# Performance work log

Measured on AMD Instinct MI355X. Metric: run time of the kernel, lower is better.

Reference implementation:

```python
import jax, jax.numpy as jnp
import numpy as np

D_MODEL = 1024
NUM_HEADS = 16
SEQ = 2048
BATCH = 4


def setup_inputs() -> dict:
    key = jax.random.key(0)
    ks = jax.random.split(key, 9)
    d = D_MODEL
    s = 0.02
    return {
        "x": jax.random.normal(ks[0], (BATCH, SEQ, d), dtype=jnp.float32),
        "WQ_w": jax.random.normal(ks[1], (d, d), dtype=jnp.float32) * s,
        "WQ_b": jnp.zeros((d,), dtype=jnp.float32),
        "WK_w": jax.random.normal(ks[2], (d, d), dtype=jnp.float32) * s,
        "WK_b": jnp.zeros((d,), dtype=jnp.float32),
        "WV_w": jax.random.normal(ks[3], (d, d), dtype=jnp.float32) * s,
        "WV_b": jnp.zeros((d,), dtype=jnp.float32),
        "WO_w": jax.random.normal(ks[4], (d, d), dtype=jnp.float32) * s,
        "WO_b": jnp.zeros((d,), dtype=jnp.float32),
    }


def reference(x, WQ_w, WQ_b, WK_w, WK_b, WV_w, WV_b, WO_w, WO_b):
    b, s, d = x.shape
    n = NUM_HEADS
    dk = d // n
    # projections (torch nn.Linear: y = x @ W.T + b)
    Q = x @ WQ_w.T + WQ_b
    K = x @ WK_w.T + WK_b
    V = x @ WV_w.T + WV_b
    # [b, s, n*dk] -> [b, n, s, dk]
    Q = Q.reshape(b, s, n, dk).transpose(0, 2, 1, 3)
    K = K.reshape(b, s, n, dk).transpose(0, 2, 1, 3)
    V = V.reshape(b, s, n, dk).transpose(0, 2, 1, 3)
    scale = 1.0 / jnp.sqrt(jnp.asarray(dk, dtype=Q.dtype))
    scores = jnp.einsum('bnqd,bnkd->bnqk', Q, K) * scale  # [b,n,s,s]
    causal = jnp.tril(jnp.ones((s, s), dtype=bool))
    scores = jnp.where(causal[None, None], scores, -jnp.inf)
    attn = jax.nn.softmax(scores, axis=-1)
    out = jnp.einsum('bnqk,bnkd->bnqd', attn, V)  # [b,n,s,dk]
    out = out.transpose(0, 2, 1, 3).reshape(b, s, d)  # merge heads
    return out @ WO_w.T + WO_b
```

## Files before the change

### kernel.cpp

```cpp
#include <hip/hip_runtime.h>
#include <hip/hip_bf16.h>
#include <stdint.h>

#define D_MODEL 1024
#define NHEAD 16
#define SEQ 2048
#define BATCH 4
#define DK 64
#define QKVSTR 3072

typedef __attribute__((ext_vector_type(8))) short short8;
typedef __attribute__((ext_vector_type(4))) float f32x4;

#if __has_builtin(__builtin_amdgcn_exp2f)
#define EXP2(x) __builtin_amdgcn_exp2f(x)
#else
#define EXP2(x) exp2f(x)
#endif

__device__ inline unsigned short f2bf(float f) {
  unsigned int u = __builtin_bit_cast(unsigned int, f);
  unsigned int r = (u + 0x7fffu + ((u >> 16) & 1u)) >> 16;
  return (unsigned short)r;
}

__device__ inline unsigned int cvt_pk_bf16(float lo, float hi) {
  unsigned int d;
  asm("v_cvt_pk_bf16_f32 %0, %1, %2" : "=v"(d) : "v"(lo), "v"(hi));
  return d;
}

#define GLOAD_LDS16(g, l) \
  __builtin_amdgcn_global_load_lds((const __attribute__((address_space(1))) unsigned int*)(g), \
      (__attribute__((address_space(3))) unsigned int*)(l), 16, 0, 0)

__global__ void cvt_kernel(const float* __restrict__ in, unsigned short* __restrict__ out, int n) {
  int i = (blockIdx.x * 256 + threadIdx.x) * 8;
  if (i >= n) return;
  const float4* p = (const float4*)(in + i);
  float4 a = p[0], b = p[1];
  union { unsigned short u[8]; uint4 v; } r;
  r.u[0] = f2bf(a.x); r.u[1] = f2bf(a.y); r.u[2] = f2bf(a.z); r.u[3] = f2bf(a.w);
  r.u[4] = f2bf(b.x); r.u[5] = f2bf(b.y); r.u[6] = f2bf(b.z); r.u[7] = f2bf(b.w);
  *(uint4*)(out + i) = r.v;
}

__global__ void cvt4_kernel(const float* __restrict__ i0, const float* __restrict__ i1,
                            const float* __restrict__ i2, const float* __restrict__ i3,
                            unsigned short* __restrict__ out, int n) {
  const int by = blockIdx.y;
  const float* in = (by == 0) ? i0 : (by == 1) ? i1 : (by == 2) ? i2 : i3;
  unsigned short* o = out + (size_t)by * n;
  int i = (blockIdx.x * 256 + threadIdx.x) * 8;
  if (i >= n) return;
  const float4* p = (const float4*)(in + i);
  float4 a = p[0], b = p[1];
  union { unsigned short u[8]; uint4 v; } r;
  r.u[0] = f2bf(a.x); r.u[1] = f2bf(a.y); r.u[2] = f2bf(a.z); r.u[3] = f2bf(a.w);
  r.u[4] = f2bf(b.x); r.u[5] = f2bf(b.y); r.u[6] = f2bf(b.z); r.u[7] = f2bf(b.w);
  *(uint4*)(o + i) = r.v;
}

template <typename CT>
__global__ __launch_bounds__(256)
void gemm_bt(const unsigned short* __restrict__ A, const unsigned short* __restrict__ B,
             const float* __restrict__ b0, const float* __restrict__ b1,
             const float* __restrict__ b2, CT* __restrict__ C, int M, int N, int K,
             int qcols, float alphaQ) {
  __shared__ unsigned short As[128 * 64];
  __shared__ unsigned short Bs[128 * 64];
  const int t = threadIdx.x;
  const int l = t & 63;
  const int w = t >> 6;
  const int wr = w >> 1, wc = w & 1;
  const int l15 = l & 15, lg = l >> 4;
  const int m0 = blockIdx.y * 128, n0 = blockIdx.x * 128;

  f32x4 acc[4][4] = {};

  const int srow = t >> 3;
  const int sc8 = t & 7;
  const int kssw = sc8 ^ (srow & 7);

  const unsigned short* ap = A + (size_t)(m0 + srow) * K + kssw * 8;
  const unsigned short* bp = B + (size_t)(n0 + srow) * K + kssw * 8;

  const int nt = K >> 6;
  for (int kt = 0; kt < nt; ++kt) {
    const int k0 = kt * 64;
    #pragma unroll
    for (int j = 0; j < 4; ++j) {
      GLOAD_LDS16(ap + (size_t)(j * 32) * K + k0, &As[(j * 32 + srow) * 64 + sc8 * 8]);
      GLOAD_LDS16(bp + (size_t)(j * 32) * K + k0, &Bs[(j * 32 + srow) * 64 + sc8 * 8]);
    }
    asm volatile("s_waitcnt vmcnt(0)" ::: "memory");
    __builtin_amdgcn_s_barrier();
    __builtin_amdgcn_sched_barrier(0);

    __builtin_amdgcn_s_setprio(1);
    #pragma unroll
    for (int kk = 0; kk < 2; ++kk) {
      short8 af[4], bfr[4];
      #pragma unroll
      for (int m = 0; m < 4; ++m) {
        int row = wr * 64 + m * 16 + l15;
        af[m] = *(const short8*)&As[row * 64 + (((kk * 4 + lg) ^ (row & 7)) * 8)];
      }
      #pragma unroll
      for (int n = 0; n < 4; ++n) {
        int row = wc * 64 + n * 16 + l15;
        bfr[n] = *(const short8*)&Bs[row * 64 + (((kk * 4 + lg) ^ (row & 7)) * 8)];
      }
      #pragma unroll
      for (int m = 0; m < 4; ++m)
        #pragma unroll
        for (int n = 0; n < 4; ++n)
          acc[m][n] = __builtin_amdgcn_mfma_f32_16x16x32_bf16(af[m], bfr[n], acc[m][n], 0, 0, 0);
    }
    __builtin_amdgcn_s_setprio(0);

    __builtin_amdgcn_s_barrier();
    __builtin_amdgcn_sched_barrier(0);
  }

  #pragma unroll
  for (int m = 0; m < 4; ++m) {
    #pragma unroll
    for (int n = 0; n < 4; ++n) {
      int col = n0 + wc * 64 + n * 16 + l15;
      const float* bp2 = (col < 1024) ? b0 : (col < 2048) ? b1 : b2;
      float bz = bp2[col & 1023];
      #pragma unroll
      for (int r = 0; r < 4; ++r) {
        int row = m0 + wr * 64 + m * 16 + lg * 4 + r;
        float v = acc[m][n][r] + bz;
        if (col < qcols) v *= alphaQ;
        if constexpr (sizeof(CT) == 2) {
          C[(size_t)row * N + col] = (CT)f2bf(v);
        } else {
          C[(size_t)row * N + col] = v;
        }
      }
    }
  }
}

__global__ __launch_bounds__(256, 3)
void attn_kernel(const unsigned short* __restrict__ QKV, unsigned short* __restrict__ AO) {
  __shared__ unsigned short Ks[2][64 * 64];
  __shared__ unsigned int Vt32[64 * 36];

  const int t = threadIdx.x;
  const int l = t & 63;
  const int w = t >> 6;
  const int l15 = l & 15, lg = l >> 4;
  const int id = blockIdx.x;
  const int qt = 31 - (id >> 6);
  const int bh = id & 63;
  const int b = bh >> 4, h = bh & 15;
  const size_t hbase = (size_t)b * SEQ * QKVSTR + h * DK;
  const size_t hbaseO = (size_t)b * SEQ * D_MODEL + h * DK;

  short8 qf[2];
  {
    const unsigned short* qp = QKV + hbase + (size_t)(qt * 64 + w * 16 + l15) * QKVSTR + lg * 8;
    qf[0] = *(const short8*)qp; qf[1] = *(const short8*)(qp + 32);
  }

  f32x4 o[4] = {};
  float lacc = 0.f;
  float m = -INFINITY;

  const int srow = t >> 3, sc8 = t & 7;
  const int kssw = sc8 ^ (srow & 7);
  const int vp_ = t & 31;
  const int vdh = (t >> 5) * 8;
  const int vpos = (vp_ & 17) | ((vp_ & 6) << 1) | ((vp_ & 8) >> 2);
  const int qrowbase = w * 16 + lg * 4;

  auto issueK = [&](int kvt, int buf) {
    const unsigned short* kp = QKV + hbase + 1024 + (size_t)(kvt * 64 + srow) * QKVSTR + kssw * 8;
    GLOAD_LDS16(kp, &Ks[buf][srow * 64 + sc8 * 8]);
    GLOAD_LDS16(kp + (size_t)32 * QKVSTR, &Ks[buf][(32 + srow) * 64 + sc8 * 8]);
  };

  const int ntiles = qt + 1;

  short8 cv0, cv1;
  issueK(0, 0);
  {
    const unsigned short* vp = QKV + hbase + 2048 + (size_t)(2 * vp_) * QKVSTR + vdh;
    cv0 = *(const short8*)vp;
    cv1 = *(const short8*)(vp + QKVSTR);
  }

  int p = 0;
  for (int kvt = 0; kvt < ntiles; ++kvt) {
    const int kv0 = kvt * 64;
    asm volatile("s_waitcnt vmcnt(0)" ::: "memory");
    __builtin_amdgcn_s_barrier();
    __builtin_amdgcn_sched_barrier(0);

    #pragma unroll
    for (int j = 0; j < 8; ++j) {
      unsigned int dw = (unsigned int)(unsigned short)cv0[j] |
                        ((unsigned int)(unsigned short)cv1[j] << 16);
      Vt32[(vdh + j) * 36 + vpos] = dw;
    }
    short8 nv0 = cv0, nv1 = cv1;
    if (kvt + 1 < ntiles) {
      issueK(kvt + 1, p ^ 1);
      const unsigned short* vp = QKV + hbase + 2048 + (size_t)(kv0 + 64 + 2 * vp_) * QKVSTR + vdh;
      nv0 = *(const short8*)vp;
      nv1 = *(const short8*)(vp + QKVSTR);
    }
    asm volatile("s_waitcnt lgkmcnt(0)" ::: "memory");
    __builtin_amdgcn_s_barrier();
    __builtin_amdgcn_sched_barrier(0);

    f32x4 s[4];
    __builtin_amdgcn_s_setprio(1);
    #pragma unroll
    for (int n = 0; n < 4; ++n) {
      int row = n * 16 + l15;
      short8 kf0 = *(const short8*)&Ks[p][row * 64 + ((lg ^ (row & 7)) * 8)];
      short8 kf1 = *(const short8*)&Ks[p][row * 64 + (((4 + lg) ^ (row & 7)) * 8)];
      f32x4 z = {};
      z = __builtin_amdgcn_mfma_f32_16x16x32_bf16(kf0, qf[0], z, 0, 0, 0);
      z = __builtin_amdgcn_mfma_f32_16x16x32_bf16(kf1, qf[1], z, 0, 0, 0);
      s[n] = z;
    }
    __builtin_amdgcn_s_setprio(0);

    short8 pa[2];
    {
      const int q = qt * 64 + w * 16 + l15;
      if (kvt == qt) {
        #pragma unroll
        for (int n = 0; n < 4; ++n)
          #pragma unroll
          for (int r = 0; r < 4; ++r)
            if (kv0 + n * 16 + lg * 4 + r > q) s[n][r] = -INFINITY;
      }
      float pm = -INFINITY;
      #pragma unroll
      for (int n = 0; n < 4; ++n)
        #pragma unroll
        for (int r = 0; r < 4; ++r) pm = fmaxf(pm, s[n][r]);
      pm = fmaxf(pm, __shfl_xor(pm, 16, 64));
      pm = fmaxf(pm, __shfl_xor(pm, 32, 64));
      float mx = fmaxf(m, pm);
      if (!__all(mx - m <= 11.0f)) {
        float al = EXP2(m - mx);
        m = mx;
        lacc *= al;
        float alo[4];
        #pragma unroll
        for (int r = 0; r < 4; ++r) alo[r] = __shfl(al, lg * 4 + r, 64);
        #pragma unroll
        for (int n = 0; n < 4; ++n)
          #pragma unroll
          for (int r = 0; r < 4; ++r) o[n][r] *= alo[r];
      }
      float ps = 0.f;
      unsigned int pw[8];
      #pragma unroll
      for (int n = 0; n < 4; ++n) {
        float p0 = EXP2(s[n][0] - m), p1 = EXP2(s[n][1] - m);
        float p2 = EXP2(s[n][2] - m), p3 = EXP2(s[n][3] - m);
        ps += (p0 + p1) + (p2 + p3);
        pw[n * 2]     = cvt_pk_bf16(p0, p1);
        pw[n * 2 + 1] = cvt_pk_bf16(p2, p3);
      }
      ps += __shfl_xor(ps, 16, 64);
      ps += __shfl_xor(ps, 32, 64);
      lacc += ps;
      uint4 u0 = make_uint4(pw[0], pw[1], pw[2], pw[3]);
      uint4 u1 = make_uint4(pw[4], pw[5], pw[6], pw[7]);
      pa[0] = __builtin_bit_cast(short8, u0);
      pa[1] = __builtin_bit_cast(short8, u1);
    }

    __builtin_amdgcn_s_setprio(1);
    #pragma unroll
    for (int n = 0; n < 4; ++n) {
      int row = n * 16 + l15;
      uint4 u0 = *(const uint4*)&Vt32[row * 36 + lg * 4];
      uint4 u1 = *(const uint4*)&Vt32[row * 36 + 16 + lg * 4];
      o[n] = __builtin_amdgcn_mfma_f32_16x16x32_bf16(pa[0], __builtin_bit_cast(short8, u0), o[n], 0, 0, 0);
      o[n] = __builtin_amdgcn_mfma_f32_16x16x32_bf16(pa[1], __builtin_bit_cast(short8, u1), o[n], 0, 0, 0);
    }
    __builtin_amdgcn_s_setprio(0);

    cv0 = nv0; cv1 = nv1;
    p ^= 1;
  }

  float inv = 1.f / lacc;
  #pragma unroll
  for (int r = 0; r < 4; ++r) {
    float iv = __shfl(inv, lg * 4 + r, 64);
    unsigned short* op = AO + hbaseO + (size_t)(qt * 64 + qrowbase + r) * D_MODEL;
    #pragma unroll
    for (int n = 0; n < 4; ++n) op[n * 16 + l15] = f2bf(o[n][r] * iv);
  }
}

extern "C" void kernel_launch(void* const* d_in, const int* in_sizes, int n_in,
                              void* d_out, int out_size, void* d_ws, size_t ws_size,
                              hipStream_t stream) {
  const float* x   = (const float*)d_in[0];
  const float* WQw = (const float*)d_in[1];
  const float* WQb = (const float*)d_in[2];
  const float* WKw = (const float*)d_in[3];
  const float* WKb = (const float*)d_in[4];
  const float* WVw = (const float*)d_in[5];
  const float* WVb = (const float*)d_in[6];
  const float* WOw = (const float*)d_in[7];
  const float* WOb = (const float*)d_in[8];
  float* out = (float*)d_out;

  const int M = BATCH * SEQ;
  const int D = D_MODEL;
  const int NX = M * D;
  const int NW = D * D;

  unsigned short* xb = (unsigned short*)d_ws;
  unsigned short* wq = xb + NX;
  unsigned short* wo = wq + 3 * NW;
  unsigned short* QKVb = wq + 4 * NW;
  unsigned short* AOb = xb;

  cvt_kernel<<<NX / 8 / 256, 256, 0, stream>>>(x, xb, NX);
  cvt4_kernel<<<dim3(NW / 8 / 256, 4), 256, 0, stream>>>(WQw, WKw, WVw, WOw, wq, NW);

  const float qscale = 0.125f * 1.4426950408889634f;
  gemm_bt<unsigned short><<<dim3(3 * D / 128, M / 128), 256, 0, stream>>>(
      xb, wq, WQb, WKb, WVb, QKVb, M, 3 * D, D, 1024, qscale);

  attn_kernel<<<2048, 256, 0, stream>>>(QKVb, AOb);

  gemm_bt<float><<<dim3(D / 128, M / 128), 256, 0, stream>>>(
      AOb, wo, WOb, WOb, WOb, out, M, D, D, 0, 1.0f);
}
```

Before: 160.5 us.

## Process two 64-row query tiles per attention block to reuse K/V loads

Each attention workgroup now handles a 128-row query block as two 64-row halves sharing the same K/V tiles staged in LDS, halving the grid to 1024 blocks. The low half skips the final KV tile, which lies past its causal diagonal. This halves K/V global loads and LDS staging per query row and amortizes barriers. In exchange it doubles accumulator and score register use per thread, which may lower occupancy under the 3-wave launch bound, and gives fewer, longer blocks for load balancing.

```diff
diff --git a/kernel.cpp b/kernel.cpp
--- a/kernel.cpp
+++ b/kernel.cpp
@@ -155,28 +155,33 @@
   const int w = t >> 6;
   const int l15 = l & 15, lg = l >> 4;
   const int id = blockIdx.x;
-  const int qt = 31 - (id >> 6);
+  const int qb = 15 - (id >> 6);
   const int bh = id & 63;
   const int b = bh >> 4, h = bh & 15;
   const size_t hbase = (size_t)b * SEQ * QKVSTR + h * DK;
   const size_t hbaseO = (size_t)b * SEQ * D_MODEL + h * DK;
 
-  short8 qf[2];
+  const int qlo = qb * 128 + w * 16;
+  const int qhi = qlo + 64;
+
+  short8 qfL[2], qfH[2];
   {
-    const unsigned short* qp = QKV + hbase + (size_t)(qt * 64 + w * 16 + l15) * QKVSTR + lg * 8;
-    qf[0] = *(const short8*)qp; qf[1] = *(const short8*)(qp + 32);
-  }
-
-  f32x4 o[4] = {};
-  float lacc = 0.f;
-  float m = -INFINITY;
+    const unsigned short* qp = QKV + hbase + (size_t)(qlo + l15) * QKVSTR + lg * 8;
+    qfL[0] = *(const short8*)qp; qfL[1] = *(const short8*)(qp + 32);
+    qp = QKV + hbase + (size_t)(qhi + l15) * QKVSTR + lg * 8;
+    qfH[0] = *(const short8*)qp; qfH[1] = *(const short8*)(qp + 32);
+  }
+
+  f32x4 oL[4] = {}, oH[4] = {};
+  float laccL = 0.f, laccH = 0.f;
+  float mL = -INFINITY, mH = -INFINITY;
 
   const int srow = t >> 3, sc8 = t & 7;
   const int kssw = sc8 ^ (srow & 7);
   const int vp_ = t & 31;
   const int vdh = (t >> 5) * 8;
   const int vpos = (vp_ & 17) | ((vp_ & 6) << 1) | ((vp_ & 8) >> 2);
-  const int qrowbase = w * 16 + lg * 4;
+  const int qrowbase = lg * 4;
 
   auto issueK = [&](int kvt, int buf) {
     const unsigned short* kp = QKV + hbase + 1024 + (size_t)(kvt * 64 + srow) * QKVSTR + kssw * 8;
@@ -184,7 +189,56 @@
     GLOAD_LDS16(kp + (size_t)32 * QKVSTR, &Ks[buf][(32 + srow) * 64 + sc8 * 8]);
   };
 
-  const int ntiles = qt + 1;
+  auto softmax_upd = [&](f32x4 (&s)[4], float& m, float& lacc, f32x4 (&o)[4],
+                         bool diag, int qbase, int kv0, short8 (&pa)[2]) {
+    if (diag) {
+      const int q = qbase + l15;
+      #pragma unroll
+      for (int n = 0; n < 4; ++n)
+        #pragma unroll
+        for (int r = 0; r < 4; ++r)
+          if (kv0 + n * 16 + lg * 4 + r > q) s[n][r] = -INFINITY;
+    }
+    float pm = -INFINITY;
+    #pragma unroll
+    for (int n = 0; n < 4; ++n)
+      #pragma unroll
+      for (int r = 0; r < 4; ++r) pm = fmaxf(pm, s[n][r]);
+    pm = fmaxf(pm, __shfl_xor(pm, 16, 64));
+    pm = fmaxf(pm, __shfl_xor(pm, 32, 64));
+    float mx = fmaxf(m, pm);
+    if (!__all(mx - m <= 11.0f)) {
+      float al = EXP2(m - mx);
+      m = mx;
+      lacc *= al;
+      float alo[4];
+      #pragma unroll
+      for (int r = 0; r < 4; ++r) alo[r] = __shfl(al, lg * 4 + r, 64);
+      #pragma unroll
+      for (int n = 0; n < 4; ++n)
+        #pragma unroll
+        for (int r = 0; r < 4; ++r) o[n][r] *= alo[r];
+    }
+    float ps = 0.f;
+    unsigned int pw[8];
+    #pragma unroll
+    for (int n = 0; n < 4; ++n) {
+      float p0 = EXP2(s[n][0] - m), p1 = EXP2(s[n][1] - m);
+      float p2 = EXP2(s[n][2] - m), p3 = EXP2(s[n][3] - m);
+      ps += (p0 + p1) + (p2 + p3);
+      pw[n * 2]     = cvt_pk_bf16(p0, p1);
+      pw[n * 2 + 1] = cvt_pk_bf16(p2, p3);
+    }
+    ps += __shfl_xor(ps, 16, 64);
+    ps += __shfl_xor(ps, 32, 64);
+    lacc += ps;
+    uint4 u0 = make_uint4(pw[0], pw[1], pw[2], pw[3]);
+    uint4 u1 = make_uint4(pw[4], pw[5], pw[6], pw[7]);
+    pa[0] = __builtin_bit_cast(short8, u0);
+    pa[1] = __builtin_bit_cast(short8, u1);
+  };
+
+  const int ntiles = 2 * qb + 2;
 
   short8 cv0, cv1;
   issueK(0, 0);
@@ -218,68 +272,31 @@
     __builtin_amdgcn_s_barrier();
     __builtin_amdgcn_sched_barrier(0);
 
-    f32x4 s[4];
+    const bool bLo = (kvt < ntiles - 1);
+    f32x4 sL[4], sH[4];
+
     __builtin_amdgcn_s_setprio(1);
     #pragma unroll
     for (int n = 0; n < 4; ++n) {
       int row = n * 16 + l15;
       short8 kf0 = *(const short8*)&Ks[p][row * 64 + ((lg ^ (row & 7)) * 8)];
       short8 kf1 = *(const short8*)&Ks[p][row * 64 + (((4 + lg) ^ (row & 7)) * 8)];
-      f32x4 z = {};
-      z = __builtin_amdgcn_mfma_f32_16x16x32_bf16(kf0, qf[0], z, 0, 0, 0);
-      z = __builtin_amdgcn_mfma_f32_16x16x32_bf16(kf1, qf[1], z, 0, 0, 0);
-      s[n] = z;
+      if (bLo) {
+        f32x4 z = {};
+        z = __builtin_amdgcn_mfma_f32_16x16x32_bf16(kf0, qfL[0], z, 0, 0, 0);
+        z = __builtin_amdgcn_mfma_f32_16x16x32_bf16(kf1, qfL[1], z, 0, 0, 0);
+        sL[n] = z;
+      }
+      f32x4 y = {};
+      y = __builtin_amdgcn_mfma_f32_16x16x32_bf16(kf0, qfH[0], y, 0, 0, 0);
+      y = __builtin_amdgcn_mfma_f32_16x16x32_bf16(kf1, qfH[1], y, 0, 0, 0);
+      sH[n] = y;
     }
     __builtin_amdgcn_s_setprio(0);
 
-    short8 pa[2];
-    {
-      const int q = qt * 64 + w * 16 + l15;
-      if (kvt == qt) {
-        #pragma unroll
-        for (int n = 0; n < 4; ++n)
-          #pragma unroll
-          for (int r = 0; r < 4; ++r)
-            if (kv0 + n * 16 + lg * 4 + r > q) s[n][r] = -INFINITY;
-      }
-      float pm = -INFINITY;
-      #pragma unroll
-      for (int n = 0; n < 4; ++n)
-        #pragma unroll
-        for (int r = 0; r < 4; ++r) pm = fmaxf(pm, s[n][r]);
-      pm = fmaxf(pm, __shfl_xor(pm, 16, 64));
-      pm = fmaxf(pm, __shfl_xor(pm, 32, 64));
-      float mx = fmaxf(m, pm);
-      if (!__all(mx - m <= 11.0f)) {
-        float al = EXP2(m - mx);
-        m = mx;
-        lacc *= al;
-        float alo[4];
-        #pragma unroll
-        for (int r = 0; r < 4; ++r) alo[r] = __shfl(al, lg * 4 + r, 64);
-        #pragma unroll
-        for (int n = 0; n < 4; ++n)
-          #pragma unroll
-          for (int r = 0; r < 4; ++r) o[n][r] *= alo[r];
-      }
-      float ps = 0.f;
-      unsigned int pw[8];
-      #pragma unroll
-      for (int n = 0; n < 4; ++n) {
-        float p0 = EXP2(s[n][0] - m), p1 = EXP2(s[n][1] - m);
-        float p2 = EXP2(s[n][2] - m), p3 = EXP2(s[n][3] - m);
-        ps += (p0 + p1) + (p2 + p3);
-        pw[n * 2]     = cvt_pk_bf16(p0, p1);
-        pw[n * 2 + 1] = cvt_pk_bf16(p2, p3);
-      }
-      ps += __shfl_xor(ps, 16, 64);
-      ps += __shfl_xor(ps, 32, 64);
-      lacc += ps;
-      uint4 u0 = make_uint4(pw[0], pw[1], pw[2], pw[3]);
-      uint4 u1 = make_uint4(pw[4], pw[5], pw[6], pw[7]);
-      pa[0] = __builtin_bit_cast(short8, u0);
-      pa[1] = __builtin_bit_cast(short8, u1);
-    }
+    short8 paL[2], paH[2];
+    if (bLo) softmax_upd(sL, mL, laccL, oL, kvt == 2 * qb, qb * 128 + w * 16, kv0, paL);
+    softmax_upd(sH, mH, laccH, oH, kvt == ntiles - 1, qhi, kv0, paH);
 
     __builtin_amdgcn_s_setprio(1);
     #pragma unroll
@@ -287,8 +304,14 @@
       int row = n * 16 + l15;
       uint4 u0 = *(const uint4*)&Vt32[row * 36 + lg * 4];
       uint4 u1 = *(const uint4*)&Vt32[row * 36 + 16 + lg * 4];
-      o[n] = __builtin_amdgcn_mfma_f32_16x16x32_bf16(pa[0], __builtin_bit_cast(short8, u0), o[n], 0, 0, 0);
-      o[n] = __builtin_amdgcn_mfma_f32_16x16x32_bf16(pa[1], __builtin_bit_cast(short8, u1), o[n], 0, 0, 0);
+      short8 vf0 = __builtin_bit_cast(short8, u0);
+      short8 vf1 = __builtin_bit_cast(short8, u1);
+      if (bLo) {
+        oL[n] = __builtin_amdgcn_mfma_f32_16x16x32_bf16(paL[0], vf0, oL[n], 0, 0, 0);
+        oL[n] = __builtin_amdgcn_mfma_f32_16x16x32_bf16(paL[1], vf1, oL[n], 0, 0, 0);
+      }
+      oH[n] = __builtin_amdgcn_mfma_f32_16x16x32_bf16(paH[0], vf0, oH[n], 0, 0, 0);
+      oH[n] = __builtin_amdgcn_mfma_f32_16x16x32_bf16(paH[1], vf1, oH[n], 0, 0, 0);
     }
     __builtin_amdgcn_s_setprio(0);
 
@@ -296,13 +319,18 @@
     p ^= 1;
   }
 
-  float inv = 1.f / lacc;
+  float invL = 1.f / laccL;
+  float invH = 1.f / laccH;
   #pragma unroll
   for (int r = 0; r < 4; ++r) {
-    float iv = __shfl(inv, lg * 4 + r, 64);
-    unsigned short* op = AO + hbaseO + (size_t)(qt * 64 + qrowbase + r) * D_MODEL;
-    #pragma unroll
-    for (int n = 0; n < 4; ++n) op[n * 16 + l15] = f2bf(o[n][r] * iv);
+    float ivL = __shfl(invL, lg * 4 + r, 64);
+    unsigned short* opL = AO + hbaseO + (size_t)(qlo + qrowbase + r) * D_MODEL;
+    #pragma unroll
+    for (int n = 0; n < 4; ++n) opL[n * 16 + l15] = f2bf(oL[n][r] * ivL);
+    float ivH = __shfl(invH, lg * 4 + r, 64);
+    unsigned short* opH = AO + hbaseO + (size_t)(qhi + qrowbase + r) * D_MODEL;
+    #pragma unroll
+    for (int n = 0; n < 4; ++n) opH[n * 16 + l15] = f2bf(oH[n][r] * ivH);
   }
 }
 
@@ -338,7 +366,7 @@
   gemm_bt<unsigned short><<<dim3(3 * D / 128, M / 128), 256, 0, stream>>>(
       xb, wq, WQb, WKb, WVb, QKVb, M, 3 * D, D, 1024, qscale);
 
-  attn_kernel<<<2048, 256, 0, stream>>>(QKVb, AOb);
+  attn_kernel<<<1024, 256, 0, stream>>>(QKVb, AOb);
 
   gemm_bt<float><<<dim3(D / 128, M / 128), 256, 0, stream>>>(
       AOb, wo, WOb, WOb, WOb, out, M, D, D, 0, 1.0f);
```

New measurement: 402.0 us. 2.5x slower.

## Switch attention to 32x32x16 MFMA with 128-row query blocks per workgroup

Applied to the files above, without the earlier changes.

Rewrites the attention kernel so each wave handles 32 query rows using 32x32x16 bf16 MFMA instead of 16x16x32, and each block covers 128 queries, which halves the grid. Every K/V tile loaded into LDS is now reused by twice as many queries. Softmax row stats need fewer cross-lane shuffles because of the transposed S layout. The cost is more accumulator registers, with occupancy lowered to 2 blocks per CU, and less parallelism and load balance with only 1024 blocks.

```diff
diff --git a/kernel.cpp b/kernel.cpp
--- a/kernel.cpp
+++ b/kernel.cpp
@@ -11,6 +11,7 @@
 
 typedef __attribute__((ext_vector_type(8))) short short8;
 typedef __attribute__((ext_vector_type(4))) float f32x4;
+typedef __attribute__((ext_vector_type(16))) float f32x16;
 
 #if __has_builtin(__builtin_amdgcn_exp2f)
 #define EXP2(x) __builtin_amdgcn_exp2f(x)
@@ -145,29 +146,34 @@
   }
 }
 
-__global__ __launch_bounds__(256, 3)
+__global__ __launch_bounds__(256, 2)
 void attn_kernel(const unsigned short* __restrict__ QKV, unsigned short* __restrict__ AO) {
   __shared__ unsigned short Ks[2][64 * 64];
-  __shared__ unsigned int Vt32[64 * 36];
+  __shared__ unsigned int Vt32[64 * 33];
 
   const int t = threadIdx.x;
   const int l = t & 63;
-  const int w = t >> 6;
-  const int l15 = l & 15, lg = l >> 4;
+  const int wave = t >> 6;
+  const int l31 = l & 31, lh = l >> 5;
   const int id = blockIdx.x;
-  const int qt = 31 - (id >> 6);
+  const int qb = 15 - (id >> 6);
   const int bh = id & 63;
   const int b = bh >> 4, h = bh & 15;
   const size_t hbase = (size_t)b * SEQ * QKVSTR + h * DK;
   const size_t hbaseO = (size_t)b * SEQ * D_MODEL + h * DK;
 
-  short8 qf[2];
+  const int q = qb * 128 + wave * 32 + l31;
+
+  short8 qf[4];
   {
-    const unsigned short* qp = QKV + hbase + (size_t)(qt * 64 + w * 16 + l15) * QKVSTR + lg * 8;
-    qf[0] = *(const short8*)qp; qf[1] = *(const short8*)(qp + 32);
-  }
-
-  f32x4 o[4] = {};
+    const unsigned short* qp = QKV + hbase + (size_t)q * QKVSTR + lh * 8;
+    qf[0] = *(const short8*)(qp);
+    qf[1] = *(const short8*)(qp + 16);
+    qf[2] = *(const short8*)(qp + 32);
+    qf[3] = *(const short8*)(qp + 48);
+  }
+
+  f32x16 o0 = {}, o1 = {};
   float lacc = 0.f;
   float m = -INFINITY;
 
@@ -175,8 +181,7 @@
   const int kssw = sc8 ^ (srow & 7);
   const int vp_ = t & 31;
   const int vdh = (t >> 5) * 8;
-  const int vpos = (vp_ & 17) | ((vp_ & 6) << 1) | ((vp_ & 8) >> 2);
-  const int qrowbase = w * 16 + lg * 4;
+  const int vpos = (vp_ & 0x19) | ((vp_ & 2) << 1) | ((vp_ & 4) >> 1);
 
   auto issueK = [&](int kvt, int buf) {
     const unsigned short* kp = QKV + hbase + 1024 + (size_t)(kvt * 64 + srow) * QKVSTR + kssw * 8;
@@ -184,7 +189,7 @@
     GLOAD_LDS16(kp + (size_t)32 * QKVSTR, &Ks[buf][(32 + srow) * 64 + sc8 * 8]);
   };
 
-  const int ntiles = qt + 1;
+  const int ntiles = 2 * qb + 2;
 
   short8 cv0, cv1;
   issueK(0, 0);
@@ -205,7 +210,7 @@
     for (int j = 0; j < 8; ++j) {
       unsigned int dw = (unsigned int)(unsigned short)cv0[j] |
                         ((unsigned int)(unsigned short)cv1[j] << 16);
-      Vt32[(vdh + j) * 36 + vpos] = dw;
+      Vt32[(vdh + j) * 33 + vpos] = dw;
     }
     short8 nv0 = cv0, nv1 = cv1;
     if (kvt + 1 < ntiles) {
@@ -218,77 +223,78 @@
     __builtin_amdgcn_s_barrier();
     __builtin_amdgcn_sched_barrier(0);
 
-    f32x4 s[4];
+    f32x16 s0 = {}, s1 = {};
     __builtin_amdgcn_s_setprio(1);
     #pragma unroll
-    for (int n = 0; n < 4; ++n) {
-      int row = n * 16 + l15;
-      short8 kf0 = *(const short8*)&Ks[p][row * 64 + ((lg ^ (row & 7)) * 8)];
-      short8 kf1 = *(const short8*)&Ks[p][row * 64 + (((4 + lg) ^ (row & 7)) * 8)];
-      f32x4 z = {};
-      z = __builtin_amdgcn_mfma_f32_16x16x32_bf16(kf0, qf[0], z, 0, 0, 0);
-      z = __builtin_amdgcn_mfma_f32_16x16x32_bf16(kf1, qf[1], z, 0, 0, 0);
-      s[n] = z;
+    for (int kg = 0; kg < 4; ++kg) {
+      int row0 = l31;
+      int row1 = 32 + l31;
+      int c = 2 * kg + lh;
+      short8 kf0 = *(const short8*)&Ks[p][row0 * 64 + ((c ^ (row0 & 7)) * 8)];
+      short8 kf1 = *(const short8*)&Ks[p][row1 * 64 + ((c ^ (row1 & 7)) * 8)];
+      s0 = __builtin_amdgcn_mfma_f32_32x32x16_bf16(kf0, qf[kg], s0, 0, 0, 0);
+      s1 = __builtin_amdgcn_mfma_f32_32x32x16_bf16(kf1, qf[kg], s1, 0, 0, 0);
     }
     __builtin_amdgcn_s_setprio(0);
 
-    short8 pa[2];
+    if (kvt >= ntiles - 2) {
+      #pragma unroll
+      for (int g = 0; g < 4; ++g)
+        #pragma unroll
+        for (int e = 0; e < 4; ++e) {
+          int kvl = 8 * g + e + 4 * lh;
+          if (kv0 + kvl > q)      s0[4 * g + e] = -INFINITY;
+          if (kv0 + 32 + kvl > q) s1[4 * g + e] = -INFINITY;
+        }
+    }
+
     {
-      const int q = qt * 64 + w * 16 + l15;
-      if (kvt == qt) {
-        #pragma unroll
-        for (int n = 0; n < 4; ++n)
-          #pragma unroll
-          for (int r = 0; r < 4; ++r)
-            if (kv0 + n * 16 + lg * 4 + r > q) s[n][r] = -INFINITY;
-      }
       float pm = -INFINITY;
       #pragma unroll
-      for (int n = 0; n < 4; ++n)
-        #pragma unroll
-        for (int r = 0; r < 4; ++r) pm = fmaxf(pm, s[n][r]);
-      pm = fmaxf(pm, __shfl_xor(pm, 16, 64));
+      for (int i = 0; i < 16; ++i) {
+        pm = fmaxf(pm, s0[i]);
+        pm = fmaxf(pm, s1[i]);
+      }
       pm = fmaxf(pm, __shfl_xor(pm, 32, 64));
       float mx = fmaxf(m, pm);
       if (!__all(mx - m <= 11.0f)) {
         float al = EXP2(m - mx);
         m = mx;
         lacc *= al;
-        float alo[4];
         #pragma unroll
-        for (int r = 0; r < 4; ++r) alo[r] = __shfl(al, lg * 4 + r, 64);
-        #pragma unroll
-        for (int n = 0; n < 4; ++n)
-          #pragma unroll
-          for (int r = 0; r < 4; ++r) o[n][r] *= alo[r];
+        for (int i = 0; i < 16; ++i) { o0[i] *= al; o1[i] *= al; }
       }
       float ps = 0.f;
-      unsigned int pw[8];
-      #pragma unroll
-      for (int n = 0; n < 4; ++n) {
-        float p0 = EXP2(s[n][0] - m), p1 = EXP2(s[n][1] - m);
-        float p2 = EXP2(s[n][2] - m), p3 = EXP2(s[n][3] - m);
-        ps += (p0 + p1) + (p2 + p3);
-        pw[n * 2]     = cvt_pk_bf16(p0, p1);
-        pw[n * 2 + 1] = cvt_pk_bf16(p2, p3);
-      }
-      ps += __shfl_xor(ps, 16, 64);
+      #pragma unroll
+      for (int i = 0; i < 16; ++i) {
+        s0[i] = EXP2(s0[i] - m); ps += s0[i];
+        s1[i] = EXP2(s1[i] - m); ps += s1[i];
+      }
       ps += __shfl_xor(ps, 32, 64);
       lacc += ps;
-      uint4 u0 = make_uint4(pw[0], pw[1], pw[2], pw[3]);
-      uint4 u1 = make_uint4(pw[4], pw[5], pw[6], pw[7]);
-      pa[0] = __builtin_bit_cast(short8, u0);
-      pa[1] = __builtin_bit_cast(short8, u1);
     }
 
     __builtin_amdgcn_s_setprio(1);
     #pragma unroll
-    for (int n = 0; n < 4; ++n) {
-      int row = n * 16 + l15;
-      uint4 u0 = *(const uint4*)&Vt32[row * 36 + lg * 4];
-      uint4 u1 = *(const uint4*)&Vt32[row * 36 + 16 + lg * 4];
-      o[n] = __builtin_amdgcn_mfma_f32_16x16x32_bf16(pa[0], __builtin_bit_cast(short8, u0), o[n], 0, 0, 0);
-      o[n] = __builtin_amdgcn_mfma_f32_16x16x32_bf16(pa[1], __builtin_bit_cast(short8, u1), o[n], 0, 0, 0);
+    for (int win = 0; win < 4; ++win) {
+      const int base = 8 * (win & 1);
+      uint4 pu;
+      if (win < 2) {
+        pu.x = cvt_pk_bf16(s0[base + 0], s0[base + 1]);
+        pu.y = cvt_pk_bf16(s0[base + 2], s0[base + 3]);
+        pu.z = cvt_pk_bf16(s0[base + 4], s0[base + 5]);
+        pu.w = cvt_pk_bf16(s0[base + 6], s0[base + 7]);
+      } else {
+        pu.x = cvt_pk_bf16(s1[base + 0], s1[base + 1]);
+        pu.y = cvt_pk_bf16(s1[base + 2], s1[base + 3]);
+        pu.z = cvt_pk_bf16(s1[base + 4], s1[base + 5]);
+        pu.w = cvt_pk_bf16(s1[base + 6], s1[base + 7]);
+      }
+      short8 pb = __builtin_bit_cast(short8, pu);
+      uint4 u0 = *(const uint4*)&Vt32[(l31) * 33 + win * 8 + lh * 4];
+      uint4 u1 = *(const uint4*)&Vt32[(32 + l31) * 33 + win * 8 + lh * 4];
+      o0 = __builtin_amdgcn_mfma_f32_32x32x16_bf16(__builtin_bit_cast(short8, u0), pb, o0, 0, 0, 0);
+      o1 = __builtin_amdgcn_mfma_f32_32x32x16_bf16(__builtin_bit_cast(short8, u1), pb, o1, 0, 0, 0);
     }
     __builtin_amdgcn_s_setprio(0);
 
@@ -297,12 +303,17 @@
   }
 
   float inv = 1.f / lacc;
+  unsigned short* op = AO + hbaseO + (size_t)q * D_MODEL;
   #pragma unroll
-  for (int r = 0; r < 4; ++r) {
-    float iv = __shfl(inv, lg * 4 + r, 64);
-    unsigned short* op = AO + hbaseO + (size_t)(qt * 64 + qrowbase + r) * D_MODEL;
-    #pragma unroll
-    for (int n = 0; n < 4; ++n) op[n * 16 + l15] = f2bf(o[n][r] * iv);
+  for (int g = 0; g < 4; ++g) {
+    int d0 = 8 * g + 4 * lh;
+    ushort4 v0, v1;
+    v0.x = f2bf(o0[4 * g + 0] * inv); v0.y = f2bf(o0[4 * g + 1] * inv);
+    v0.z = f2bf(o0[4 * g + 2] * inv); v0.w = f2bf(o0[4 * g + 3] * inv);
+    v1.x = f2bf(o1[4 * g + 0] * inv); v1.y = f2bf(o1[4 * g + 1] * inv);
+    v1.z = f2bf(o1[4 * g + 2] * inv); v1.w = f2bf(o1[4 * g + 3] * inv);
+    *(ushort4*)(op + d0) = v0;
+    *(ushort4*)(op + 32 + d0) = v1;
   }
 }
 
@@ -338,7 +349,7 @@
   gemm_bt<unsigned short><<<dim3(3 * D / 128, M / 128), 256, 0, stream>>>(
       xb, wq, WQb, WKb, WVb, QKVb, M, 3 * D, D, 1024, qscale);
 
-  attn_kernel<<<2048, 256, 0, stream>>>(QKVb, AOb);
+  attn_kernel<<<1024, 256, 0, stream>>>(QKVb, AOb);
 
   gemm_bt<float><<<dim3(D / 128, M / 128), 256, 0, stream>>>(
       AOb, wo, WOb, WOb, WOb, out, M, D, D, 0, 1.0f);
```

Measured after the change: 157.3 us. 1.02x faster.
